# Performance work log

Measured on AMD Instinct MI355X. Metric: run time of the kernel, lower is better.

Reference implementation:

```python
import jax, jax.numpy as jnp
import numpy as np
import math

# Module constants derived from init_kwargs
DIM1, DIM2 = 32, 32          # n_patches = (512//16, 512//16)
PREFIX = 8                   # num_prefix_tokens
STD = 5.0                    # gauss_std
NUM_HEADS = 12               # orig_attn.num_heads (ViT-B)
EMBED_DIM = 768


def gaussian_window(n1, n2, std):
    # torch linspace(start*c, (start+(n-1))*c, n) == (arange(n)-(n-1)/2)*c
    c = 1.0 / (std * math.sqrt(2.0))
    k1 = (jnp.arange(n1, dtype=jnp.float32) - (n1 - 1) / 2.0) * c
    k2 = (jnp.arange(n2, dtype=jnp.float32) - (n2 - 1) / 2.0) * c
    return jnp.exp(-(k1[:, None] ** 2 + k2[None, :] ** 2))


def attn_addition():
    # Same-padding cross-correlation of per-token delta images with the window
    # collapses to: add[(i,l),(p,q)] = window[i-p+DIM1-1, l-q+DIM2-1]
    win = gaussian_window(2 * DIM1 - 1, 2 * DIM2 - 1, STD)
    i = jnp.arange(DIM1)
    l = jnp.arange(DIM2)
    di = i[:, None] - i[None, :] + (DIM1 - 1)   # [i, p]
    dl = l[:, None] - l[None, :] + (DIM2 - 1)   # [l, q]
    add = win[di[:, None, :, None], dl[None, :, None, :]]  # [i, l, p, q]
    add = add.reshape(DIM1 * DIM2, DIM1 * DIM2)
    # zero rows/cols for prefix tokens (prepended)
    return jnp.pad(add, ((PREFIX, 0), (PREFIX, 0)))


def setup_inputs() -> dict:
    key = jax.random.key(0)
    ks = jax.random.split(key, 5)
    B, N, C = 8, DIM1 * DIM2 + PREFIX, EMBED_DIM
    return {
        "x": jax.random.normal(ks[0], (B, N, C), dtype=jnp.float32),
        "qkv_w": jax.random.normal(ks[1], (3 * C, C), dtype=jnp.float32) * 0.02,
        "qkv_b": jax.random.normal(ks[2], (3 * C,), dtype=jnp.float32) * 0.02,
        "proj_w": jax.random.normal(ks[3], (C, C), dtype=jnp.float32) * 0.02,
        "proj_b": jax.random.normal(ks[4], (C,), dtype=jnp.float32) * 0.02,
    }


def reference(x, qkv_w, qkv_b, proj_w, proj_b):
    B, N, C = x.shape
    H = NUM_HEADS
    hd = C // H
    scale = hd ** (-0.5)
    add = attn_addition()  # [N, N] constant bias

    qkv = x @ qkv_w.T + qkv_b                      # [B, N, 3C]
    q, k, v = jnp.split(qkv, 3, axis=-1)           # q computed but unused (k.k^T attention)
    k = k.reshape(B, N, H, hd)
    v = v.reshape(B, N, H, hd)

    attn = jnp.einsum("bihd,bjhd->bhij", k, k) * scale + add[None, None]
    attn = jax.nn.softmax(attn, axis=-1)
    out = jnp.einsum("bhij,bjhd->bihd", attn, v).reshape(B, N, C)
    out = out @ proj_w.T + proj_b
    return out
```

## Files before the change

kernel.cpp:

```cpp
#include <hip/hip_runtime.h>
#include <stdint.h>

typedef __bf16 bf16;
typedef _Float16 f16;
typedef __bf16 bf16x8 __attribute__((ext_vector_type(8)));
typedef __bf16 bf16x4 __attribute__((ext_vector_type(4)));
typedef float f32x4 __attribute__((ext_vector_type(4)));
typedef _Float16 f16x4 __attribute__((ext_vector_type(4)));

#define NSEQ 1032
#define BATCH 8
#define NHEADS 12
#define HD 64
#define CDIM 768
#define MROWS (BATCH * NSEQ)
#define PREFIX 8
#define NJT 17
#define NQ16 72
#define KSCALE 0.42466090f

__device__ __forceinline__ unsigned short f2bf_rne(float f) {
    union { float f; uint32_t u; } v; v.f = f;
    uint32_t u = v.u;
    return (unsigned short)((u + 0x7fffu + ((u >> 16) & 1u)) >> 16);
}

__device__ __forceinline__ void gload_lds16(const bf16* g, bf16* l) {
    __builtin_amdgcn_global_load_lds(
        (const __attribute__((address_space(1))) void*)g,
        (__attribute__((address_space(3))) void*)l, 16, 0, 0);
}

__device__ __forceinline__ void cast4(const float* src, bf16* dst, int i) {
    float4 f = ((const float4*)src)[i];
    ushort4 o;
    o.x = f2bf_rne(f.x); o.y = f2bf_rne(f.y);
    o.z = f2bf_rne(f.z); o.w = f2bf_rne(f.w);
    ((ushort4*)dst)[i] = o;
}

__device__ __forceinline__ void bar() {
    asm volatile("s_waitcnt lgkmcnt(0)" ::: "memory");
    __builtin_amdgcn_s_barrier();
    asm volatile("" ::: "memory");
}

__global__ void prep_kernel(const float* __restrict__ x,
                            const float* __restrict__ wkv,
                            const float* __restrict__ pw,
                            bf16* __restrict__ x_bf, bf16* __restrict__ wkv_bf,
                            bf16* __restrict__ pw_bf, f16* __restrict__ Bias) {
    const int N0 = NQ16 * NJT * 1024;
    const int N1 = MROWS * CDIM / 4;
    const int N2 = 2 * CDIM * CDIM / 4;
    const int N3 = CDIM * CDIM / 4;
    int i = blockIdx.x * blockDim.x + threadIdx.x;
    if (i < N0) {
        int r    = i & 3;
        int l15  = (i >> 2) & 15;
        int quad = (i >> 6) & 3;
        int kt   = (i >> 8) & 3;
        int rest = i >> 10;
        int q16  = rest / NJT;
        int jt   = rest - q16 * NJT;
        int q = q16 * 16 + l15;
        int k = jt * 64 + kt * 16 + quad * 4 + r;
        float v;
        if (k >= NSEQ) v = -65504.f;
        else if (q < PREFIX || q >= NSEQ || k < PREFIX) v = 0.f;
        else {
            int rp = q - PREFIX, cp = k - PREFIX;
            int d1 = (rp >> 5) - (cp >> 5);
            int d2 = (rp & 31) - (cp & 31);
            v = 1.44269504f * __expf(-0.02f * (float)(d1 * d1 + d2 * d2));
        }
        Bias[i] = (f16)v;
        return;
    }
    i -= N0;
    if (i < N1) { cast4(x, x_bf, i); return; }
    i -= N1;
    if (i < N2) { cast4(wkv, wkv_bf, i); return; }
    i -= N2;
    if (i < N3) { cast4(pw, pw_bf, i); }
}

template<int EPI>
__global__ __launch_bounds__(256) void gemm_nt(
    const bf16* __restrict__ A, const bf16* __restrict__ B,
    const float* __restrict__ bias,
    float* __restrict__ Cout, bf16* __restrict__ Kout, bf16* __restrict__ Vout,
    int M, int N, int K)
{
    __shared__ bf16 sA[128 * 32];
    __shared__ bf16 sB[128 * 32];
    const int t = threadIdx.x;
    const int w = t >> 6;
    const int l = t & 63;
    const int quad = l >> 4;
    const int l15 = l & 15;
    const int wy = w >> 1, wx = w & 1;
    const int m0 = blockIdx.y * 128;
    const int n0 = blockIdx.x * 128;
    const int co = (quad ^ ((l15 >> 1) & 3)) * 8;

    int r0 = t >> 2,          c0 = (t & 3) ^ ((r0 >> 1) & 3);
    int r1 = (t + 256) >> 2,  c1 = ((t + 256) & 3) ^ ((r1 >> 1) & 3);
    int ra0 = m0 + r0; if (ra0 >= M) ra0 = M - 1;
    int ra1 = m0 + r1; if (ra1 >= M) ra1 = M - 1;
    const bf16* gA0 = A + (size_t)ra0 * K + c0 * 8;
    const bf16* gA1 = A + (size_t)ra1 * K + c1 * 8;
    const bf16* gB0 = B + (size_t)(n0 + r0) * K + c0 * 8;
    const bf16* gB1 = B + (size_t)(n0 + r1) * K + c1 * 8;
    bf16* dA0 = &sA[(size_t)(w * 64) * 8];
    bf16* dA1 = &sA[(size_t)(256 + w * 64) * 8];
    bf16* dB0 = &sB[(size_t)(w * 64) * 8];
    bf16* dB1 = &sB[(size_t)(256 + w * 64) * 8];

    f32x4 acc[4][4] = {};

    for (int k0 = 0; k0 < K; k0 += 32) {
        __syncthreads();
        gload_lds16(gA0, dA0); gload_lds16(gA1, dA1);
        gload_lds16(gB0, dB0); gload_lds16(gB1, dB1);
        gA0 += 32; gA1 += 32; gB0 += 32; gB1 += 32;
        __syncthreads();
        bf16x8 af[4], bq[4];
        #pragma unroll
        for (int mt = 0; mt < 4; ++mt)
            af[mt] = *(const bf16x8*)&sA[(wy*64 + mt*16 + l15) * 32 + co];
        #pragma unroll
        for (int nt = 0; nt < 4; ++nt)
            bq[nt] = *(const bf16x8*)&sB[(wx*64 + nt*16 + l15) * 32 + co];
        #pragma unroll
        for (int mt = 0; mt < 4; ++mt)
            #pragma unroll
            for (int nt = 0; nt < 4; ++nt)
                acc[mt][nt] = __builtin_amdgcn_mfma_f32_16x16x32_bf16(af[mt], bq[nt], acc[mt][nt], 0, 0, 0);
    }

    if (EPI == 0) {
        #pragma unroll
        for (int mt = 0; mt < 4; ++mt) {
            #pragma unroll
            for (int r = 0; r < 4; ++r) {
                int m = m0 + wy*64 + mt*16 + quad*4 + r;
                if (m >= M) continue;
                #pragma unroll
                for (int nt = 0; nt < 4; ++nt) {
                    int n = n0 + wx*64 + nt*16 + l15;
                    Cout[(size_t)m * N + n] = acc[mt][nt][r] + bias[n];
                }
            }
        }
    } else {
        #pragma unroll
        for (int mt = 0; mt < 4; ++mt) {
            int mb = m0 + wy*64 + mt*16 + quad*4;
            if (mb >= M) continue;
            int b = mb / NSEQ, s = mb % NSEQ;
            #pragma unroll
            for (int nt = 0; nt < 4; ++nt) {
                int n = n0 + wx*64 + nt*16 + l15;
                float bn = bias[n];
                if (n < CDIM) {
                    int h = n >> 6, d = n & 63;
                    bf16* kp = &Kout[(((size_t)(b*NHEADS + h))*NSEQ + s)*HD + d];
                    #pragma unroll
                    for (int r = 0; r < 4; ++r)
                        kp[(size_t)r * HD] = (bf16)((acc[mt][nt][r] + bn) * KSCALE);
                } else {
                    int n2 = n - CDIM;
                    int h = n2 >> 6, d = n2 & 63;
                    bf16x4 pv = { (bf16)(acc[mt][nt][0] + bn), (bf16)(acc[mt][nt][1] + bn),
                                  (bf16)(acc[mt][nt][2] + bn), (bf16)(acc[mt][nt][3] + bn) };
                    *(bf16x4*)&Vout[(((size_t)(b*NHEADS + h))*HD + d)*NSEQ + s] = pv;
                }
            }
        }
    }
}

__global__ __launch_bounds__(256) void attn_kernel(
    const bf16* __restrict__ Kbuf, const bf16* __restrict__ VTbuf,
    const f16* __restrict__ Bias, bf16* __restrict__ Hout)
{
    const int bh = blockIdx.x;
    const int b = bh / NHEADS, h = bh % NHEADS;
    const int q0 = blockIdx.y * 128;
    const bf16* Kh  = Kbuf  + (size_t)bh * NSEQ * HD;
    const bf16* VTh = VTbuf + (size_t)bh * NSEQ * HD;

    __shared__ bf16 sK[64 * 64];
    __shared__ bf16 sVT[64 * 64];
    __shared__ bf16 sP[128 * 64];
    __shared__ float sL[128];

    const int t = threadIdx.x;
    const int w = t >> 6, l = t & 63, quad = l >> 4, l15 = l & 15;
    const int sw = l15 & 7;

    const int r0 = t >> 3, c0 = t & 7;
    const int r1 = r0 + 32;
    bf16* dK0 = &sK [r0*64 + ((c0 ^ (r0 & 7)) << 3)];
    bf16* dK1 = &sK [r1*64 + ((c0 ^ (r1 & 7)) << 3)];
    bf16* dV0 = &sVT[r0*64 + ((c0 ^ (r0 & 7)) << 3)];
    bf16* dV1 = &sVT[r1*64 + ((c0 ^ (r1 & 7)) << 3)];

    const f16* bq0 = Bias + ((size_t)(blockIdx.y*8 + w*2 + 0) * NJT) * 1024 + quad*64 + l15*4;
    const f16* bq1 = Bias + ((size_t)(blockIdx.y*8 + w*2 + 1) * NJT) * 1024 + quad*64 + l15*4;

    bf16x8 qf[2][2];
    int qrow[2];
    #pragma unroll
    for (int qh = 0; qh < 2; ++qh) {
        qrow[qh] = q0 + w*32 + qh*16 + l15;
        int row = qrow[qh] > NSEQ - 1 ? NSEQ - 1 : qrow[qh];
        #pragma unroll
        for (int ks = 0; ks < 2; ++ks)
            qf[qh][ks] = *(const bf16x8*)&Kh[(size_t)row * HD + ks*32 + quad*8];
    }

    f32x4 Oacc[2][4] = {};
    float ps[2] = {0.f, 0.f};
    const int sPr0 = (w*32 + l15) * 64;

    uint4 kva, kvb, vva, vvb;
    f16x4 bpf[2][4];
#define PREFETCH(J, JT) do { \
        int ka_ = (J) + r0; if (ka_ > NSEQ-1) ka_ = NSEQ-1; \
        int kb_ = (J) + r1; if (kb_ > NSEQ-1) kb_ = NSEQ-1; \
        int ja_ = (J) + c0*8; if (ja_ > NSEQ-8) ja_ = NSEQ-8; \
        kva = *(const uint4*)&Kh [(size_t)ka_ * HD + c0*8]; \
        kvb = *(const uint4*)&Kh [(size_t)kb_ * HD + c0*8]; \
        vva = *(const uint4*)&VTh[(size_t)r0 * NSEQ + ja_]; \
        vvb = *(const uint4*)&VTh[(size_t)r1 * NSEQ + ja_]; \
        _Pragma("unroll") \
        for (int kt = 0; kt < 4; ++kt) { \
            bpf[0][kt] = *(const f16x4*)(bq0 + (size_t)(JT)*1024 + kt*256); \
            bpf[1][kt] = *(const f16x4*)(bq1 + (size_t)(JT)*1024 + kt*256); \
        } \
    } while (0)

    PREFETCH(0, 0);

    for (int jt = 0; jt < NJT; ++jt) {
        *(uint4*)dK0 = kva; *(uint4*)dK1 = kvb;
        *(uint4*)dV0 = vva; *(uint4*)dV1 = vvb;

        f32x4 sacc[2][4];
        #pragma unroll
        for (int qh = 0; qh < 2; ++qh)
            #pragma unroll
            for (int kt = 0; kt < 4; ++kt)
                sacc[qh][kt] = (f32x4){(float)bpf[qh][kt].x, (float)bpf[qh][kt].y,
                                       (float)bpf[qh][kt].z, (float)bpf[qh][kt].w};

        int jn  = (jt == NJT-1) ? 0 : (jt+1) * 64;
        int jtn = (jt == NJT-1) ? 0 : jt+1;
        PREFETCH(jn, jtn);

        bar();

        #pragma unroll
        for (int ks = 0; ks < 2; ++ks) {
            bf16x8 af[4];
            #pragma unroll
            for (int kt = 0; kt < 4; ++kt) {
                int row = kt*16 + l15;
                af[kt] = *(const bf16x8*)&sK[row*64 + (((ks*4 + quad) ^ (row & 7)) << 3)];
            }
            __builtin_amdgcn_s_setprio(1);
            #pragma unroll
            for (int qh = 0; qh < 2; ++qh)
                #pragma unroll
                for (int kt = 0; kt < 4; ++kt)
                    sacc[qh][kt] = __builtin_amdgcn_mfma_f32_16x16x32_bf16(
                        af[kt], qf[qh][ks], sacc[qh][kt], 0, 0, 0);
            __builtin_amdgcn_s_setprio(0);
        }

        #pragma unroll
        for (int qh = 0; qh < 2; ++qh)
            #pragma unroll
            for (int kt = 0; kt < 4; ++kt) {
                float p0 = __builtin_exp2f(sacc[qh][kt][0]);
                float p1 = __builtin_exp2f(sacc[qh][kt][1]);
                float p2 = __builtin_exp2f(sacc[qh][kt][2]);
                float p3 = __builtin_exp2f(sacc[qh][kt][3]);
                ps[qh] += (p0 + p1) + (p2 + p3);
                bf16x4 pv = { (bf16)p0, (bf16)p1, (bf16)p2, (bf16)p3 };
                int g = (kt*2 + (quad >> 1)) ^ sw;
                *(bf16x4*)&sP[sPr0 + qh*1024 + g*8 + (quad & 1)*4] = pv;
            }

        #pragma unroll
        for (int ks = 0; ks < 2; ++ks) {
            bf16x8 bv[4];
            #pragma unroll
            for (int dt = 0; dt < 4; ++dt) {
                int row = dt*16 + l15;
                bv[dt] = *(const bf16x8*)&sVT[row*64 + (((ks*4 + quad) ^ (row & 7)) << 3)];
            }
            __builtin_amdgcn_s_setprio(1);
            #pragma unroll
            for (int qh = 0; qh < 2; ++qh) {
                bf16x8 ap = *(const bf16x8*)&sP[sPr0 + qh*1024 + (((ks*4 + quad) ^ sw) * 8)];
                #pragma unroll
                for (int dt = 0; dt < 4; ++dt)
                    Oacc[qh][dt] = __builtin_amdgcn_mfma_f32_16x16x32_bf16(
                        ap, bv[dt], Oacc[qh][dt], 0, 0, 0);
            }
            __builtin_amdgcn_s_setprio(0);
        }

        bar();
    }
#undef PREFETCH

    #pragma unroll
    for (int qh = 0; qh < 2; ++qh) {
        float s = ps[qh];
        s += __shfl_xor(s, 16, 64);
        s += __shfl_xor(s, 32, 64);
        if (l < 16) sL[w*32 + qh*16 + l] = s;
    }

    #pragma unroll
    for (int qh = 0; qh < 2; ++qh)
        #pragma unroll
        for (int r = 0; r < 4; ++r) {
            int g = q0 + w*32 + qh*16 + quad*4 + r;
            if (g >= NSEQ) continue;
            float inv = 1.f / sL[w*32 + qh*16 + quad*4 + r];
            size_t base = ((size_t)(b * NSEQ) + g) * CDIM + h * HD;
            #pragma unroll
            for (int dt = 0; dt < 4; ++dt)
                Hout[base + dt*16 + l15] = (bf16)(Oacc[qh][dt][r] * inv);
        }
}

extern "C" void kernel_launch(void* const* d_in, const int* in_sizes, int n_in,
                              void* d_out, int out_size, void* d_ws, size_t ws_size,
                              hipStream_t stream) {
    const float* x      = (const float*)d_in[0];
    const float* qkv_w  = (const float*)d_in[1];
    const float* qkv_b  = (const float*)d_in[2];
    const float* proj_w = (const float*)d_in[3];
    const float* proj_b = (const float*)d_in[4];
    float* out = (float*)d_out;

    char* ws = (char*)d_ws;
    const size_t XBF_BYTES   = (size_t)MROWS * CDIM * 2;
    const size_t WKV_BYTES   = (size_t)2 * CDIM * CDIM * 2;
    const size_t PW_BYTES    = (size_t)CDIM * CDIM * 2;
    const size_t KBF_BYTES   = (size_t)BATCH * NHEADS * NSEQ * HD * 2;

    bf16* x_bf   = (bf16*)ws;
    bf16* wkv_bf = (bf16*)(ws + XBF_BYTES);
    bf16* pw_bf  = (bf16*)(ws + XBF_BYTES + WKV_BYTES);
    bf16* k_bf   = (bf16*)(ws + XBF_BYTES + WKV_BYTES + PW_BYTES);
    bf16* vt_bf  = (bf16*)(ws + XBF_BYTES + WKV_BYTES + PW_BYTES + KBF_BYTES);
    f16*  bias_t = (f16*)(ws + XBF_BYTES + WKV_BYTES + PW_BYTES + KBF_BYTES + KBF_BYTES);

    {
        int total = NQ16 * NJT * 1024 + MROWS * CDIM / 4
                  + 2 * CDIM * CDIM / 4 + CDIM * CDIM / 4;
        prep_kernel<<<dim3((total + 255) / 256), dim3(256), 0, stream>>>(
            x, qkv_w + (size_t)CDIM * CDIM, proj_w, x_bf, wkv_bf, pw_bf, bias_t);
    }

    {
        dim3 grid(1536 / 128, (MROWS + 127) / 128);
        gemm_nt<1><<<grid, dim3(256), 0, stream>>>(x_bf, wkv_bf, qkv_b + CDIM,
                                                   nullptr, k_bf, vt_bf,
                                                   MROWS, 1536, CDIM);
    }

    {
        dim3 grid(BATCH * NHEADS, (NSEQ + 127) / 128);
        attn_kernel<<<grid, dim3(256), 0, stream>>>(k_bf, vt_bf, bias_t, x_bf);
    }

    {
        dim3 grid(CDIM / 128, (MROWS + 127) / 128);
        gemm_nt<0><<<grid, dim3(256), 0, stream>>>(x_bf, pw_bf, proj_b,
                                                   out, nullptr, nullptr,
                                                   MROWS, CDIM, CDIM);
    }
}
```

Before: 238.4 us.

## Double-buffer K/V in LDS, pad K/V buffers, fp32 bias, MFMA row sums

The attention kernel now double-buffers K and V^T tiles in shared memory and unrolls the tile loop in pairs, so staging the next tile no longer needs a trailing barrier. K and V^T buffers are padded to 1152 rows and the padding is zeroed in the prep kernel, which removes the clamping arithmetic from the prefetch path. The bias table is stored as fp32, dropping the f16-to-f32 conversion but doubling bias read traffic. Softmax row sums are computed with an extra MFMA against a ones vector instead of scalar adds plus shuffles and an LDS reduction. The price is more LDS, extra MFMA work, and relying on exp2 of the -65504 bias to zero out the padded keys.

```diff
diff --git a/kernel.cpp b/kernel.cpp
--- a/kernel.cpp
+++ b/kernel.cpp
@@ -6,7 +6,6 @@
 typedef __bf16 bf16x8 __attribute__((ext_vector_type(8)));
 typedef __bf16 bf16x4 __attribute__((ext_vector_type(4)));
 typedef float f32x4 __attribute__((ext_vector_type(4)));
-typedef _Float16 f16x4 __attribute__((ext_vector_type(4)));
 
 #define NSEQ 1032
 #define BATCH 8
@@ -17,6 +16,8 @@
 #define PREFIX 8
 #define NJT 17
 #define NQ16 72
+#define KSTRIDE 1152
+#define VSTRIDE 1152
 #define KSCALE 0.42466090f
 
 __device__ __forceinline__ unsigned short f2bf_rne(float f) {
@@ -49,11 +50,14 @@
                             const float* __restrict__ wkv,
                             const float* __restrict__ pw,
                             bf16* __restrict__ x_bf, bf16* __restrict__ wkv_bf,
-                            bf16* __restrict__ pw_bf, f16* __restrict__ Bias) {
+                            bf16* __restrict__ pw_bf, float* __restrict__ Bias,
+                            bf16* __restrict__ k_bf, bf16* __restrict__ vt_bf) {
     const int N0 = NQ16 * NJT * 1024;
     const int N1 = MROWS * CDIM / 4;
     const int N2 = 2 * CDIM * CDIM / 4;
     const int N3 = CDIM * CDIM / 4;
+    const int N4 = BATCH * NHEADS * 120 * 8;
+    const int N5 = BATCH * NHEADS * 64 * 15;
     int i = blockIdx.x * blockDim.x + threadIdx.x;
     if (i < N0) {
         int r    = i & 3;
@@ -74,7 +78,7 @@
             int d2 = (rp & 31) - (cp & 31);
             v = 1.44269504f * __expf(-0.02f * (float)(d1 * d1 + d2 * d2));
         }
-        Bias[i] = (f16)v;
+        Bias[i] = v;
         return;
     }
     i -= N0;
@@ -82,7 +86,22 @@
     i -= N1;
     if (i < N2) { cast4(wkv, wkv_bf, i); return; }
     i -= N2;
-    if (i < N3) { cast4(pw, pw_bf, i); }
+    if (i < N3) { cast4(pw, pw_bf, i); return; }
+    i -= N3;
+    if (i < N4) {
+        int bh = i / 960, rem = i - bh * 960;
+        int row = 1032 + (rem >> 3), ch = rem & 7;
+        uint4 z = {0u, 0u, 0u, 0u};
+        *(uint4*)&k_bf[((size_t)bh * KSTRIDE + row) * HD + ch * 8] = z;
+        return;
+    }
+    i -= N4;
+    if (i < N5) {
+        int bh = i / 960, rem = i - bh * 960;
+        int d = rem / 15, ch = rem - d * 15;
+        uint4 z = {0u, 0u, 0u, 0u};
+        *(uint4*)&vt_bf[((size_t)bh * HD + d) * VSTRIDE + 1032 + ch * 8] = z;
+    }
 }
 
 template<int EPI>
@@ -165,7 +184,7 @@
                 float bn = bias[n];
                 if (n < CDIM) {
                     int h = n >> 6, d = n & 63;
-                    bf16* kp = &Kout[(((size_t)(b*NHEADS + h))*NSEQ + s)*HD + d];
+                    bf16* kp = &Kout[(((size_t)(b*NHEADS + h))*KSTRIDE + s)*HD + d];
                     #pragma unroll
                     for (int r = 0; r < 4; ++r)
                         kp[(size_t)r * HD] = (bf16)((acc[mt][nt][r] + bn) * KSCALE);
@@ -174,7 +193,7 @@
                     int h = n2 >> 6, d = n2 & 63;
                     bf16x4 pv = { (bf16)(acc[mt][nt][0] + bn), (bf16)(acc[mt][nt][1] + bn),
                                   (bf16)(acc[mt][nt][2] + bn), (bf16)(acc[mt][nt][3] + bn) };
-                    *(bf16x4*)&Vout[(((size_t)(b*NHEADS + h))*HD + d)*NSEQ + s] = pv;
+                    *(bf16x4*)&Vout[(((size_t)(b*NHEADS + h))*HD + d)*VSTRIDE + s] = pv;
                 }
             }
         }
@@ -183,18 +202,17 @@
 
 __global__ __launch_bounds__(256) void attn_kernel(
     const bf16* __restrict__ Kbuf, const bf16* __restrict__ VTbuf,
-    const f16* __restrict__ Bias, bf16* __restrict__ Hout)
+    const float* __restrict__ Bias, bf16* __restrict__ Hout)
 {
     const int bh = blockIdx.x;
     const int b = bh / NHEADS, h = bh % NHEADS;
     const int q0 = blockIdx.y * 128;
-    const bf16* Kh  = Kbuf  + (size_t)bh * NSEQ * HD;
-    const bf16* VTh = VTbuf + (size_t)bh * NSEQ * HD;
-
-    __shared__ bf16 sK[64 * 64];
-    __shared__ bf16 sVT[64 * 64];
+    const bf16* Kh  = Kbuf  + (size_t)bh * KSTRIDE * HD;
+    const bf16* VTh = VTbuf + (size_t)bh * HD * VSTRIDE;
+
+    __shared__ bf16 sK[2][64 * 64];
+    __shared__ bf16 sVT[2][64 * 64];
     __shared__ bf16 sP[128 * 64];
-    __shared__ float sL[128];
 
     const int t = threadIdx.x;
     const int w = t >> 6, l = t & 63, quad = l >> 4, l15 = l & 15;
@@ -202,129 +220,116 @@
 
     const int r0 = t >> 3, c0 = t & 7;
     const int r1 = r0 + 32;
-    bf16* dK0 = &sK [r0*64 + ((c0 ^ (r0 & 7)) << 3)];
-    bf16* dK1 = &sK [r1*64 + ((c0 ^ (r1 & 7)) << 3)];
-    bf16* dV0 = &sVT[r0*64 + ((c0 ^ (r0 & 7)) << 3)];
-    bf16* dV1 = &sVT[r1*64 + ((c0 ^ (r1 & 7)) << 3)];
-
-    const f16* bq0 = Bias + ((size_t)(blockIdx.y*8 + w*2 + 0) * NJT) * 1024 + quad*64 + l15*4;
-    const f16* bq1 = Bias + ((size_t)(blockIdx.y*8 + w*2 + 1) * NJT) * 1024 + quad*64 + l15*4;
+    const int dk0 = r0*64 + ((c0 ^ (r0 & 7)) << 3);
+    const int dk1 = r1*64 + ((c0 ^ (r1 & 7)) << 3);
+
+    const bf16* pK0 = Kh + (size_t)r0 * HD + c0 * 8;
+    const bf16* pK1 = Kh + (size_t)r1 * HD + c0 * 8;
+    const bf16* pV0 = VTh + (size_t)r0 * VSTRIDE + c0 * 8;
+    const bf16* pV1 = VTh + (size_t)r1 * VSTRIDE + c0 * 8;
+    const float* pB0 = Bias + ((size_t)(blockIdx.y*8 + w*2 + 0) * NJT) * 1024 + quad*64 + l15*4;
+    const float* pB1 = Bias + ((size_t)(blockIdx.y*8 + w*2 + 1) * NJT) * 1024 + quad*64 + l15*4;
 
     bf16x8 qf[2][2];
-    int qrow[2];
     #pragma unroll
     for (int qh = 0; qh < 2; ++qh) {
-        qrow[qh] = q0 + w*32 + qh*16 + l15;
-        int row = qrow[qh] > NSEQ - 1 ? NSEQ - 1 : qrow[qh];
+        int row = q0 + w*32 + qh*16 + l15;
         #pragma unroll
         for (int ks = 0; ks < 2; ++ks)
             qf[qh][ks] = *(const bf16x8*)&Kh[(size_t)row * HD + ks*32 + quad*8];
     }
 
+    bf16x8 onesb;
+    #pragma unroll
+    for (int e = 0; e < 8; ++e) onesb[e] = (bf16)1.0f;
+
     f32x4 Oacc[2][4] = {};
-    float ps[2] = {0.f, 0.f};
+    f32x4 Lacc[2] = {};
     const int sPr0 = (w*32 + l15) * 64;
 
     uint4 kva, kvb, vva, vvb;
-    f16x4 bpf[2][4];
-#define PREFETCH(J, JT) do { \
-        int ka_ = (J) + r0; if (ka_ > NSEQ-1) ka_ = NSEQ-1; \
-        int kb_ = (J) + r1; if (kb_ > NSEQ-1) kb_ = NSEQ-1; \
-        int ja_ = (J) + c0*8; if (ja_ > NSEQ-8) ja_ = NSEQ-8; \
-        kva = *(const uint4*)&Kh [(size_t)ka_ * HD + c0*8]; \
-        kvb = *(const uint4*)&Kh [(size_t)kb_ * HD + c0*8]; \
-        vva = *(const uint4*)&VTh[(size_t)r0 * NSEQ + ja_]; \
-        vvb = *(const uint4*)&VTh[(size_t)r1 * NSEQ + ja_]; \
+    f32x4 bpf[2][4];
+
+#define PREFETCH() do { \
+        kva = *(const uint4*)pK0; kvb = *(const uint4*)pK1; \
+        vva = *(const uint4*)pV0; vvb = *(const uint4*)pV1; \
+        pK0 += 64*HD; pK1 += 64*HD; pV0 += 64; pV1 += 64; \
         _Pragma("unroll") \
         for (int kt = 0; kt < 4; ++kt) { \
-            bpf[0][kt] = *(const f16x4*)(bq0 + (size_t)(JT)*1024 + kt*256); \
-            bpf[1][kt] = *(const f16x4*)(bq1 + (size_t)(JT)*1024 + kt*256); \
+            bpf[0][kt] = *(const f32x4*)(pB0 + kt*256); \
+            bpf[1][kt] = *(const f32x4*)(pB1 + kt*256); \
+        } \
+        pB0 += 1024; pB1 += 1024; \
+    } while (0)
+
+#define ITER(CUR) do { \
+        *(uint4*)&sK[CUR][dk0] = kva; *(uint4*)&sK[CUR][dk1] = kvb; \
+        *(uint4*)&sVT[CUR][dk0] = vva; *(uint4*)&sVT[CUR][dk1] = vvb; \
+        f32x4 sacc[2][4]; \
+        _Pragma("unroll") \
+        for (int qh = 0; qh < 2; ++qh) \
+            _Pragma("unroll") \
+            for (int kt = 0; kt < 4; ++kt) \
+                sacc[qh][kt] = bpf[qh][kt]; \
+        PREFETCH(); \
+        bar(); \
+        _Pragma("unroll") \
+        for (int ks = 0; ks < 2; ++ks) { \
+            bf16x8 af[4]; \
+            _Pragma("unroll") \
+            for (int kt = 0; kt < 4; ++kt) \
+                af[kt] = *(const bf16x8*)&sK[CUR][(kt*16 + l15)*64 + (((ks*4 + quad) ^ sw) << 3)]; \
+            __builtin_amdgcn_s_setprio(1); \
+            _Pragma("unroll") \
+            for (int qh = 0; qh < 2; ++qh) \
+                _Pragma("unroll") \
+                for (int kt = 0; kt < 4; ++kt) \
+                    sacc[qh][kt] = __builtin_amdgcn_mfma_f32_16x16x32_bf16( \
+                        af[kt], qf[qh][ks], sacc[qh][kt], 0, 0, 0); \
+            __builtin_amdgcn_s_setprio(0); \
+        } \
+        _Pragma("unroll") \
+        for (int qh = 0; qh < 2; ++qh) \
+            _Pragma("unroll") \
+            for (int kt = 0; kt < 4; ++kt) { \
+                float p0 = __builtin_exp2f(sacc[qh][kt][0]); \
+                float p1 = __builtin_exp2f(sacc[qh][kt][1]); \
+                float p2 = __builtin_exp2f(sacc[qh][kt][2]); \
+                float p3 = __builtin_exp2f(sacc[qh][kt][3]); \
+                bf16x4 pv = { (bf16)p0, (bf16)p1, (bf16)p2, (bf16)p3 }; \
+                int g = (kt*2 + (quad >> 1)) ^ sw; \
+                *(bf16x4*)&sP[sPr0 + qh*1024 + g*8 + (quad & 1)*4] = pv; \
+            } \
+        _Pragma("unroll") \
+        for (int ks = 0; ks < 2; ++ks) { \
+            bf16x8 bv[4]; \
+            _Pragma("unroll") \
+            for (int dt = 0; dt < 4; ++dt) \
+                bv[dt] = *(const bf16x8*)&sVT[CUR][(dt*16 + l15)*64 + (((ks*4 + quad) ^ sw) << 3)]; \
+            __builtin_amdgcn_s_setprio(1); \
+            _Pragma("unroll") \
+            for (int qh = 0; qh < 2; ++qh) { \
+                bf16x8 ap = *(const bf16x8*)&sP[sPr0 + qh*1024 + (((ks*4 + quad) ^ sw) * 8)]; \
+                _Pragma("unroll") \
+                for (int dt = 0; dt < 4; ++dt) \
+                    Oacc[qh][dt] = __builtin_amdgcn_mfma_f32_16x16x32_bf16( \
+                        ap, bv[dt], Oacc[qh][dt], 0, 0, 0); \
+                Lacc[qh] = __builtin_amdgcn_mfma_f32_16x16x32_bf16( \
+                    ap, onesb, Lacc[qh], 0, 0, 0); \
+            } \
+            __builtin_amdgcn_s_setprio(0); \
         } \
     } while (0)
 
-    PREFETCH(0, 0);
-
-    for (int jt = 0; jt < NJT; ++jt) {
-        *(uint4*)dK0 = kva; *(uint4*)dK1 = kvb;
-        *(uint4*)dV0 = vva; *(uint4*)dV1 = vvb;
-
-        f32x4 sacc[2][4];
-        #pragma unroll
-        for (int qh = 0; qh < 2; ++qh)
-            #pragma unroll
-            for (int kt = 0; kt < 4; ++kt)
-                sacc[qh][kt] = (f32x4){(float)bpf[qh][kt].x, (float)bpf[qh][kt].y,
-                                       (float)bpf[qh][kt].z, (float)bpf[qh][kt].w};
-
-        int jn  = (jt == NJT-1) ? 0 : (jt+1) * 64;
-        int jtn = (jt == NJT-1) ? 0 : jt+1;
-        PREFETCH(jn, jtn);
-
-        bar();
-
-        #pragma unroll
-        for (int ks = 0; ks < 2; ++ks) {
-            bf16x8 af[4];
-            #pragma unroll
-            for (int kt = 0; kt < 4; ++kt) {
-                int row = kt*16 + l15;
-                af[kt] = *(const bf16x8*)&sK[row*64 + (((ks*4 + quad) ^ (row & 7)) << 3)];
-            }
-            __builtin_amdgcn_s_setprio(1);
-            #pragma unroll
-            for (int qh = 0; qh < 2; ++qh)
-                #pragma unroll
-                for (int kt = 0; kt < 4; ++kt)
-                    sacc[qh][kt] = __builtin_amdgcn_mfma_f32_16x16x32_bf16(
-                        af[kt], qf[qh][ks], sacc[qh][kt], 0, 0, 0);
-            __builtin_amdgcn_s_setprio(0);
-        }
-
-        #pragma unroll
-        for (int qh = 0; qh < 2; ++qh)
-            #pragma unroll
-            for (int kt = 0; kt < 4; ++kt) {
-                float p0 = __builtin_exp2f(sacc[qh][kt][0]);
-                float p1 = __builtin_exp2f(sacc[qh][kt][1]);
-                float p2 = __builtin_exp2f(sacc[qh][kt][2]);
-                float p3 = __builtin_exp2f(sacc[qh][kt][3]);
-                ps[qh] += (p0 + p1) + (p2 + p3);
-                bf16x4 pv = { (bf16)p0, (bf16)p1, (bf16)p2, (bf16)p3 };
-                int g = (kt*2 + (quad >> 1)) ^ sw;
-                *(bf16x4*)&sP[sPr0 + qh*1024 + g*8 + (quad & 1)*4] = pv;
-            }
-
-        #pragma unroll
-        for (int ks = 0; ks < 2; ++ks) {
-            bf16x8 bv[4];
-            #pragma unroll
-            for (int dt = 0; dt < 4; ++dt) {
-                int row = dt*16 + l15;
-                bv[dt] = *(const bf16x8*)&sVT[row*64 + (((ks*4 + quad) ^ (row & 7)) << 3)];
-            }
-            __builtin_amdgcn_s_setprio(1);
-            #pragma unroll
-            for (int qh = 0; qh < 2; ++qh) {
-                bf16x8 ap = *(const bf16x8*)&sP[sPr0 + qh*1024 + (((ks*4 + quad) ^ sw) * 8)];
-                #pragma unroll
-                for (int dt = 0; dt < 4; ++dt)
-                    Oacc[qh][dt] = __builtin_amdgcn_mfma_f32_16x16x32_bf16(
-                        ap, bv[dt], Oacc[qh][dt], 0, 0, 0);
-            }
-            __builtin_amdgcn_s_setprio(0);
-        }
-
-        bar();
-    }
+    PREFETCH();
+    ITER(0);
+    #pragma unroll 1
+    for (int it = 0; it < (NJT - 1) / 2; ++it) {
+        ITER(1);
+        ITER(0);
+    }
+#undef ITER
 #undef PREFETCH
-
-    #pragma unroll
-    for (int qh = 0; qh < 2; ++qh) {
-        float s = ps[qh];
-        s += __shfl_xor(s, 16, 64);
-        s += __shfl_xor(s, 32, 64);
-        if (l < 16) sL[w*32 + qh*16 + l] = s;
-    }
 
     #pragma unroll
     for (int qh = 0; qh < 2; ++qh)
@@ -332,7 +337,7 @@
         for (int r = 0; r < 4; ++r) {
             int g = q0 + w*32 + qh*16 + quad*4 + r;
             if (g >= NSEQ) continue;
-            float inv = 1.f / sL[w*32 + qh*16 + quad*4 + r];
+            float inv = 1.f / Lacc[qh][r];
             size_t base = ((size_t)(b * NSEQ) + g) * CDIM + h * HD;
             #pragma unroll
             for (int dt = 0; dt < 4; ++dt)
@@ -354,20 +359,23 @@
     const size_t XBF_BYTES   = (size_t)MROWS * CDIM * 2;
     const size_t WKV_BYTES   = (size_t)2 * CDIM * CDIM * 2;
     const size_t PW_BYTES    = (size_t)CDIM * CDIM * 2;
-    const size_t KBF_BYTES   = (size_t)BATCH * NHEADS * NSEQ * HD * 2;
-
-    bf16* x_bf   = (bf16*)ws;
-    bf16* wkv_bf = (bf16*)(ws + XBF_BYTES);
-    bf16* pw_bf  = (bf16*)(ws + XBF_BYTES + WKV_BYTES);
-    bf16* k_bf   = (bf16*)(ws + XBF_BYTES + WKV_BYTES + PW_BYTES);
-    bf16* vt_bf  = (bf16*)(ws + XBF_BYTES + WKV_BYTES + PW_BYTES + KBF_BYTES);
-    f16*  bias_t = (f16*)(ws + XBF_BYTES + WKV_BYTES + PW_BYTES + KBF_BYTES + KBF_BYTES);
+    const size_t BIAS_BYTES  = (size_t)NQ16 * NJT * 1024 * 4;
+    const size_t KBF_BYTES   = (size_t)BATCH * NHEADS * KSTRIDE * HD * 2;
+
+    bf16*  x_bf   = (bf16*)ws;
+    bf16*  wkv_bf = (bf16*)(ws + XBF_BYTES);
+    bf16*  pw_bf  = (bf16*)(ws + XBF_BYTES + WKV_BYTES);
+    float* bias_t = (float*)(ws + XBF_BYTES + WKV_BYTES + PW_BYTES);
+    bf16*  k_bf   = (bf16*)(ws + XBF_BYTES + WKV_BYTES + PW_BYTES + BIAS_BYTES);
+    bf16*  vt_bf  = (bf16*)(ws + XBF_BYTES + WKV_BYTES + PW_BYTES + BIAS_BYTES + KBF_BYTES);
 
     {
         int total = NQ16 * NJT * 1024 + MROWS * CDIM / 4
-                  + 2 * CDIM * CDIM / 4 + CDIM * CDIM / 4;
+                  + 2 * CDIM * CDIM / 4 + CDIM * CDIM / 4
+                  + BATCH * NHEADS * 120 * 8 + BATCH * NHEADS * 64 * 15;
         prep_kernel<<<dim3((total + 255) / 256), dim3(256), 0, stream>>>(
-            x, qkv_w + (size_t)CDIM * CDIM, proj_w, x_bf, wkv_bf, pw_bf, bias_t);
+            x, qkv_w + (size_t)CDIM * CDIM, proj_w, x_bf, wkv_bf, pw_bf, bias_t,
+            k_bf, vt_bf);
     }
 
     {
```

Measured after the change: 227.5 us. 4.6% less time.
